# Kernel optimization log

Measured on AMD Instinct MI355X. Metric: run time of the kernel, lower is better.

Reference implementation:

```python
import jax, jax.numpy as jnp
import numpy as np

N_HEAD = 16
D_MODEL = 1024


def setup_inputs() -> dict:
    key = jax.random.key(0)
    ks = jax.random.split(key, 12)
    B, S, D = 2, 2048, D_MODEL
    s = 0.02
    return {
        "q": jax.random.normal(ks[0], (B, S, D), jnp.float32),
        "k": jax.random.normal(ks[1], (B, S, D), jnp.float32),
        "v": jax.random.normal(ks[2], (B, S, 2 * D), jnp.float32),
        "Wq": jax.random.normal(ks[3], (D, D), jnp.float32) * s,
        "bq": jnp.zeros((D,), jnp.float32),
        "Wk": jax.random.normal(ks[4], (D, D), jnp.float32) * s,
        "bk": jnp.zeros((D,), jnp.float32),
        "Wv": jax.random.normal(ks[5], (2 * D, D), jnp.float32) * s,
        "bv": jnp.zeros((D,), jnp.float32),
        "Wfc": jax.random.normal(ks[6], (D, 2 * D), jnp.float32) * s,
        "bfc": jnp.zeros((2 * D,), jnp.float32),
        "padding_mask": jnp.ones((B, S), jnp.int32),
    }


def reference(q, k, v, Wq, bq, Wk, bk, Wv, bv, Wfc, bfc, padding_mask):
    B, S, D = q.shape
    H = N_HEAD
    dh = D // H
    scale = jnp.float32(np.sqrt(dh))
    # projections, split heads -> [B, H, S, dh]
    qh = (q @ Wq + bq).reshape(B, S, H, dh).transpose(0, 2, 1, 3)
    kh = (k @ Wk + bk).reshape(B, S, H, dh).transpose(0, 2, 1, 3)
    vh = (v @ Wv + bv).reshape(B, S, H, dh).transpose(0, 2, 1, 3)
    # scores [B, H, S, S]
    attn = jnp.einsum("bhqd,bhkd->bhqk", qh, kh) / scale
    pad = (padding_mask == 0)[:, None, None, :]  # [B,1,1,S]
    attn = jnp.where(pad, -jnp.inf, attn)
    attn = jax.nn.softmax(attn, axis=-1)
    # dropout p=0 in eval -> identity
    out = jnp.einsum("bhqk,bhkd->bhqd", attn, vh)
    out = out.transpose(0, 2, 1, 3).reshape(B, S, D)
    out = out @ Wfc + bfc  # [B, S, 2D]
    attn_avg = attn.sum(axis=1) / H  # [B, S, S]
    return out, attn_avg
```

## Files before the change

### kernel.cpp

```cpp
#include <hip/hip_runtime.h>
#include <math.h>

#define BATCH   2
#define SLEN    2048
#define DMODEL  1024
#define NHEAD   16
#define DHEAD   64
#define DOUT    2048
#define MROWS   (BATCH * SLEN)
#define NSPLIT  2
#define KSPAN   (SLEN / NSPLIT)

typedef short bf16x8 __attribute__((ext_vector_type(8)));
typedef float floatx4 __attribute__((ext_vector_type(4)));

static __device__ __forceinline__ unsigned short f2bf(float f) {
  unsigned u = __float_as_uint(f);
  u += 0x7fff + ((u >> 16) & 1);
  return (unsigned short)(u >> 16);
}
static __device__ __forceinline__ float bf2f(unsigned short s) {
  return __uint_as_float(((unsigned)s) << 16);
}
static __device__ __forceinline__ unsigned int pk_bf16(float a, float b) {
#if defined(__gfx950__) && __has_builtin(__builtin_amdgcn_cvt_pk_bf16_f32)
  typedef __bf16 bf2_t __attribute__((ext_vector_type(2)));
  bf2_t r = __builtin_amdgcn_cvt_pk_bf16_f32(a, b);
  return __builtin_bit_cast(unsigned int, r);
#else
  return ((unsigned)f2bf(b) << 16) | f2bf(a);
#endif
}
static __device__ __forceinline__ floatx4 mfma16(bf16x8 a, bf16x8 b, floatx4 c) {
  return __builtin_amdgcn_mfma_f32_16x16x32_bf16(a, b, c, 0, 0, 0);
}
static __device__ __forceinline__ void gll16(const void* g, void* l) {
  __builtin_amdgcn_global_load_lds(
      (const __attribute__((address_space(1))) unsigned int*)g,
      (__attribute__((address_space(3))) unsigned int*)l, 16, 0, 0);
}

__global__ __launch_bounds__(256) void conv_all_k(
    const float* __restrict__ q, const float* __restrict__ k,
    const float* __restrict__ v, unsigned short* __restrict__ qb,
    unsigned short* __restrict__ kb, unsigned short* __restrict__ vb) {
  int i = blockIdx.x * 256 + threadIdx.x;
  const float* src;
  unsigned short* dst;
  if (i < (1 << 19)) { src = q; dst = qb; }
  else if (i < (1 << 20)) { src = k; dst = kb; i -= 1 << 19; }
  else { src = v; dst = vb; i -= 1 << 20; }
  const float4 a = ((const float4*)src)[i * 2];
  const float4 b = ((const float4*)src)[i * 2 + 1];
  uint4 u;
  u.x = pk_bf16(a.x, a.y);
  u.y = pk_bf16(a.z, a.w);
  u.z = pk_bf16(b.x, b.y);
  u.w = pk_bf16(b.z, b.w);
  ((uint4*)dst)[i] = u;
}

__global__ __launch_bounds__(256) void wtrans_all_k(
    const float* __restrict__ Wq, const float* __restrict__ Wk,
    const float* __restrict__ Wv, const float* __restrict__ Wfc,
    unsigned short* __restrict__ WqT, unsigned short* __restrict__ WkT,
    unsigned short* __restrict__ WvT, unsigned short* __restrict__ WfcT) {
  __shared__ float T[32][33];
  int id = blockIdx.x;
  const float* W;
  unsigned short* WT;
  int K, N;
  if (id < 1024)      { W = Wq;  WT = WqT;  K = 1024; N = 1024; }
  else if (id < 2048) { W = Wk;  WT = WkT;  K = 1024; N = 1024; id -= 1024; }
  else if (id < 4096) { W = Wv;  WT = WvT;  K = 2048; N = 1024; id -= 2048; }
  else                { W = Wfc; WT = WfcT; K = 1024; N = 2048; id -= 4096; }
  const int ntn = N / 32;
  const int n0 = (id % ntn) * 32, k0 = (id / ntn) * 32;
  const int t = threadIdx.x;
  {
    const int r = t >> 3, c4 = (t & 7) * 4;
    const float4 w = *(const float4*)(W + (size_t)(k0 + r) * N + n0 + c4);
    T[r][c4 + 0] = w.x; T[r][c4 + 1] = w.y; T[r][c4 + 2] = w.z; T[r][c4 + 3] = w.w;
  }
  __syncthreads();
  {
    const int n = t >> 3, k4 = (t & 7) * 4;
    uint2 u;
    u.x = pk_bf16(T[k4 + 0][n], T[k4 + 1][n]);
    u.y = pk_bf16(T[k4 + 2][n], T[k4 + 3][n]);
    *(uint2*)(WT + (size_t)(n0 + n) * K + k0 + k4) = u;
  }
}

template <int MODE>
static __device__ __forceinline__ void gemm_body(
    const unsigned short* __restrict__ A, const unsigned short* __restrict__ BT,
    const float* __restrict__ bias, void* __restrict__ C, int M, int K, int N,
    int row0, int col0) {
  __shared__ unsigned short As[128 * 64];
  __shared__ unsigned short Bs[64 * 64];
  const int t = threadIdx.x;
  const int w = t >> 6, l = t & 63, quad = l >> 4, lq = l & 15;
  const int wm = (w >> 1) * 64, wn = (w & 1) * 32;

  const unsigned short* aS[4];
#pragma unroll
  for (int jj = 0; jj < 4; jj++) {
    const int m = (w * 4 + jj) * 8 + (l >> 3);
    aS[jj] = A + (size_t)(row0 + m) * K + (((l & 7) ^ (m & 7)) << 3);
  }
  const unsigned short* bS[2];
#pragma unroll
  for (int jj = 0; jj < 2; jj++) {
    const int n = (w * 2 + jj) * 8 + (l >> 3);
    bS[jj] = BT + (size_t)(col0 + n) * K + (((l & 7) ^ (n & 7)) << 3);
  }

  floatx4 acc[4][2];
#pragma unroll
  for (int i = 0; i < 4; i++)
#pragma unroll
    for (int j = 0; j < 2; j++) acc[i][j] = (floatx4){0.f, 0.f, 0.f, 0.f};

  for (int kt = 0; kt < K; kt += 64) {
#pragma unroll
    for (int jj = 0; jj < 4; jj++)
      gll16(aS[jj] + kt, As + (w * 4 + jj) * 512);
#pragma unroll
    for (int jj = 0; jj < 2; jj++)
      gll16(bS[jj] + kt, Bs + (w * 2 + jj) * 512);
    __syncthreads();

    bf16x8 af[4][2], bfr[2][2];
#pragma unroll
    for (int ti = 0; ti < 4; ti++) {
      const int m = wm + ti * 16 + lq;
#pragma unroll
      for (int h = 0; h < 2; h++)
        af[ti][h] = *(const bf16x8*)(As + m * 64 + (((h * 4 + quad) ^ (m & 7)) << 3));
    }
#pragma unroll
    for (int tj = 0; tj < 2; tj++) {
      const int n = wn + tj * 16 + lq;
#pragma unroll
      for (int h = 0; h < 2; h++)
        bfr[tj][h] = *(const bf16x8*)(Bs + n * 64 + (((h * 4 + quad) ^ (n & 7)) << 3));
    }
#pragma unroll
    for (int ti = 0; ti < 4; ti++)
#pragma unroll
      for (int tj = 0; tj < 2; tj++) {
        acc[ti][tj] = mfma16(af[ti][0], bfr[tj][0], acc[ti][tj]);
        acc[ti][tj] = mfma16(af[ti][1], bfr[tj][1], acc[ti][tj]);
      }
    __syncthreads();
  }

#pragma unroll
  for (int tj = 0; tj < 2; tj++) {
    const int col = col0 + wn + tj * 16 + lq;
    const float bv = bias[col];
    if (MODE == 2) {
#pragma unroll
      for (int ti = 0; ti < 4; ti++) {
        uint2 u;
        u.x = pk_bf16(acc[ti][tj][0] + bv, acc[ti][tj][1] + bv);
        u.y = pk_bf16(acc[ti][tj][2] + bv, acc[ti][tj][3] + bv);
        *(uint2*)((unsigned short*)C + (size_t)col * M + row0 + wm + ti * 16 +
                  quad * 4) = u;
      }
    } else {
#pragma unroll
      for (int ti = 0; ti < 4; ti++)
#pragma unroll
        for (int r = 0; r < 4; r++) {
          const int row = row0 + wm + ti * 16 + quad * 4 + r;
          const float vv = acc[ti][tj][r] + bv;
          if (MODE == 1)
            ((float*)C)[(size_t)row * N + col] = vv;
          else
            ((unsigned short*)C)[(size_t)row * N + col] = f2bf(vv);
        }
    }
  }
}

__global__ __launch_bounds__(256) void proj_k(
    const unsigned short* qb, const unsigned short* kb, const unsigned short* vb,
    const unsigned short* WqT, const unsigned short* WkT,
    const unsigned short* WvT, const float* bq, const float* bk,
    const float* bv, unsigned short* Qp, unsigned short* Kp,
    unsigned short* VT) {
  const int z = blockIdx.z;
  if (z == 2)
    gemm_body<2>(vb, WvT, bv, VT, MROWS, 2 * DMODEL, DMODEL,
                 blockIdx.y * 128, blockIdx.x * 64);
  else if (z == 1)
    gemm_body<0>(kb, WkT, bk, Kp, MROWS, DMODEL, DMODEL,
                 blockIdx.y * 128, blockIdx.x * 64);
  else
    gemm_body<0>(qb, WqT, bq, Qp, MROWS, DMODEL, DMODEL,
                 blockIdx.y * 128, blockIdx.x * 64);
}
__global__ __launch_bounds__(256) void fc_k(
    const unsigned short* att, const unsigned short* WfcT, const float* bfc,
    float* out) {
  gemm_body<1>(att, WfcT, bfc, out, MROWS, DMODEL, DOUT,
               blockIdx.y * 128, blockIdx.x * 64);
}

__global__ __launch_bounds__(256) void flash_mfma_k(
    const unsigned short* __restrict__ Qp, const unsigned short* __restrict__ Kp,
    const unsigned short* __restrict__ VT, const int* __restrict__ mask,
    unsigned short* __restrict__ Opart, float* __restrict__ Lpart) {
  __shared__ unsigned short Ks[64 * 64];
  __shared__ unsigned short Vs[64 * 64];
  __shared__ unsigned short Ps[4][16 * 68];
  __shared__ float biasL[KSPAN];
  const int t = threadIdx.x;
  const int w = t >> 6, l = t & 63, quad = l >> 4, lq = l & 15;
  const int q0 = blockIdx.x * 64;
  const int h = blockIdx.y >> 1, split = blockIdx.y & 1;
  const int b = blockIdx.z;

  for (int i = t; i < KSPAN; i += 256)
    biasL[i] = mask[b * SLEN + split * KSPAN + i] ? 0.f : -INFINITY;

  const unsigned short* qptr =
      Qp + (size_t)(b * SLEN + q0 + w * 16 + lq) * DMODEL + h * 64;
  const bf16x8 aq0 = *(const bf16x8*)(qptr + quad * 8);
  const bf16x8 aq1 = *(const bf16x8*)(qptr + 32 + quad * 8);

  int krow[2], kchunk[2];
#pragma unroll
  for (int jj = 0; jj < 2; jj++) {
    krow[jj] = (w * 2 + jj) * 8 + (l >> 3);
    kchunk[jj] = (l & 7) ^ (krow[jj] & 7);
  }
  const unsigned short* Kbase = Kp + (size_t)b * SLEN * DMODEL + h * 64;
  const unsigned short* Vbase = VT + (size_t)h * 64 * MROWS + b * SLEN;

  floatx4 acc_o[4];
#pragma unroll
  for (int dj = 0; dj < 4; dj++) acc_o[dj] = (floatx4){0.f, 0.f, 0.f, 0.f};
  float lsum = 0.f;
  unsigned short* PsW = &Ps[w][0];

  for (int k0s = 0; k0s < KSPAN; k0s += 64) {
    const int k0 = split * KSPAN + k0s;
    __syncthreads();
#pragma unroll
    for (int jj = 0; jj < 2; jj++) {
      const int inst = w * 2 + jj;
      gll16(Kbase + (size_t)(k0 + krow[jj]) * DMODEL + kchunk[jj] * 8,
            Ks + inst * 512);
      gll16(Vbase + (size_t)krow[jj] * MROWS + k0 + kchunk[jj] * 8,
            Vs + inst * 512);
    }
    __syncthreads();

#pragma unroll
    for (int ti = 0; ti < 4; ti++) {
      const int kk = ti * 16 + lq;
      const bf16x8 bk0 = *(const bf16x8*)(Ks + kk * 64 + ((quad ^ (kk & 7)) << 3));
      const bf16x8 bk1 =
          *(const bf16x8*)(Ks + kk * 64 + (((4 + quad) ^ (kk & 7)) << 3));
      floatx4 z = (floatx4){0.f, 0.f, 0.f, 0.f};
      z = mfma16(bk0, aq0, z);
      z = mfma16(bk1, aq1, z);
      const float4 bb = *(const float4*)&biasL[k0s + ti * 16 + quad * 4];
      const float e0 = __expf(fmaf(z[0], 0.125f, bb.x));
      const float e1 = __expf(fmaf(z[1], 0.125f, bb.y));
      const float e2 = __expf(fmaf(z[2], 0.125f, bb.z));
      const float e3 = __expf(fmaf(z[3], 0.125f, bb.w));
      lsum += (e0 + e1) + (e2 + e3);
      uint2 pk;
      pk.x = pk_bf16(e0, e1);
      pk.y = pk_bf16(e2, e3);
      *(uint2*)(PsW + lq * 68 + ti * 16 + quad * 4) = pk;
    }
    __asm__ __volatile__("" ::: "memory");
    const bf16x8 ap0 = *(const bf16x8*)(PsW + lq * 68 + quad * 8);
    const bf16x8 ap1 = *(const bf16x8*)(PsW + lq * 68 + 32 + quad * 8);
#pragma unroll
    for (int dj = 0; dj < 4; dj++) {
      const int d = dj * 16 + lq;
      const bf16x8 bv0 = *(const bf16x8*)(Vs + d * 64 + ((quad ^ (d & 7)) << 3));
      const bf16x8 bv1 =
          *(const bf16x8*)(Vs + d * 64 + (((4 + quad) ^ (d & 7)) << 3));
      acc_o[dj] = mfma16(ap0, bv0, acc_o[dj]);
      acc_o[dj] = mfma16(ap1, bv1, acc_o[dj]);
    }
  }

  lsum += __shfl_xor(lsum, 16);
  lsum += __shfl_xor(lsum, 32);

  const size_t obase =
      (((size_t)split * BATCH + b) * NHEAD + h) * SLEN + q0 + w * 16;
#pragma unroll
  for (int dj = 0; dj < 4; dj++)
#pragma unroll
    for (int r = 0; r < 4; r++)
      Opart[(obase + quad * 4 + r) * DHEAD + dj * 16 + lq] = f2bf(acc_o[dj][r]);
  if (quad == 0) Lpart[obase + lq] = lsum;
}

__global__ __launch_bounds__(256) void combine_k(
    const unsigned short* __restrict__ Opart, const float* __restrict__ Lpart,
    unsigned short* __restrict__ att, float* __restrict__ lbuf) {
  const int gid = blockIdx.x * 256 + threadIdx.x;
  const int row = gid >> 3;
  const int d8 = (gid & 7) * 8;
  const float l0 = Lpart[row];
  const float l1 = Lpart[(size_t)BATCH * NHEAD * SLEN + row];
  const float lt = l0 + l1;
  const float il = (lt > 0.f) ? 1.f / lt : 0.f;
  const bf16x8 o0 = *(const bf16x8*)(Opart + (size_t)row * DHEAD + d8);
  const bf16x8 o1 = *(const bf16x8*)(Opart + (size_t)(BATCH * NHEAD * SLEN) * DHEAD +
                                     (size_t)row * DHEAD + d8);
  const int b = row >> 15, hh = (row >> 11) & 15, q = row & 2047;
  unsigned short* dst = att + (size_t)(b * SLEN + q) * DMODEL + hh * 64 + d8;
  float vv[8];
#pragma unroll
  for (int j = 0; j < 8; j++)
    vv[j] = (bf2f((unsigned short)o0[j]) + bf2f((unsigned short)o1[j])) * il;
  uint4 u;
  u.x = pk_bf16(vv[0], vv[1]);
  u.y = pk_bf16(vv[2], vv[3]);
  u.z = pk_bf16(vv[4], vv[5]);
  u.w = pk_bf16(vv[6], vv[7]);
  *(uint4*)dst = u;
  if ((gid & 7) == 0) lbuf[row] = lt;
}

__global__ __launch_bounds__(256) void attn_avg_mfma_k(
    const unsigned short* __restrict__ Qp, const unsigned short* __restrict__ Kp,
    const float* __restrict__ lbuf, const int* __restrict__ mask,
    float* __restrict__ aout) {
  __shared__ unsigned short Ks[64 * 64];
  __shared__ float ilL[NHEAD * 64];
  const int t = threadIdx.x;
  const int w = t >> 6, l = t & 63, quad = l >> 4, lq = l & 15;
  const int k0 = blockIdx.x * 64, q0 = blockIdx.y * 64, b = blockIdx.z;

  for (int i = t; i < NHEAD * 64; i += 256) {
    const float lv = lbuf[(b * NHEAD + (i >> 6)) * SLEN + q0 + (i & 63)];
    ilL[i] = (lv > 0.f) ? 1.f / lv : 0.f;
  }
  float bb[4];
#pragma unroll
  for (int ti = 0; ti < 4; ti++)
    bb[ti] = mask[b * SLEN + k0 + ti * 16 + lq] ? 0.f : -INFINITY;

  floatx4 acc[4];
#pragma unroll
  for (int ti = 0; ti < 4; ti++) acc[ti] = (floatx4){0.f, 0.f, 0.f, 0.f};

  int krow[2], kchunk[2];
#pragma unroll
  for (int jj = 0; jj < 2; jj++) {
    krow[jj] = (w * 2 + jj) * 8 + (l >> 3);
    kchunk[jj] = (l & 7) ^ (krow[jj] & 7);
  }
  const unsigned short* Kbase = Kp + (size_t)(b * SLEN + k0) * DMODEL;
  const unsigned short* qbase =
      Qp + (size_t)(b * SLEN + q0 + w * 16 + lq) * DMODEL;

  for (int h = 0; h < NHEAD; h++) {
    __syncthreads();
#pragma unroll
    for (int jj = 0; jj < 2; jj++)
      gll16(Kbase + (size_t)krow[jj] * DMODEL + h * 64 + kchunk[jj] * 8,
            Ks + (w * 2 + jj) * 512);
    __syncthreads();

    const bf16x8 aq0 = *(const bf16x8*)(qbase + h * 64 + quad * 8);
    const bf16x8 aq1 = *(const bf16x8*)(qbase + h * 64 + 32 + quad * 8);
    const float4 il4 = *(const float4*)&ilL[h * 64 + w * 16 + quad * 4];
    const float ila[4] = {il4.x, il4.y, il4.z, il4.w};
#pragma unroll
    for (int ti = 0; ti < 4; ti++) {
      const int kk = ti * 16 + lq;
      const bf16x8 bk0 = *(const bf16x8*)(Ks + kk * 64 + ((quad ^ (kk & 7)) << 3));
      const bf16x8 bk1 =
          *(const bf16x8*)(Ks + kk * 64 + (((4 + quad) ^ (kk & 7)) << 3));
      floatx4 z = (floatx4){0.f, 0.f, 0.f, 0.f};
      z = mfma16(aq0, bk0, z);
      z = mfma16(aq1, bk1, z);
#pragma unroll
      for (int r = 0; r < 4; r++)
        acc[ti][r] = fmaf(__expf(fmaf(z[r], 0.125f, bb[ti])), ila[r], acc[ti][r]);
    }
  }
  const float ih = 1.f / NHEAD;
#pragma unroll
  for (int ti = 0; ti < 4; ti++)
#pragma unroll
    for (int r = 0; r < 4; r++)
      aout[(size_t)(b * SLEN + q0 + w * 16 + quad * 4 + r) * SLEN + k0 +
           ti * 16 + lq] = acc[ti][r] * ih;
}

extern "C" void kernel_launch(void* const* d_in, const int* in_sizes, int n_in,
                              void* d_out, int out_size, void* d_ws, size_t ws_size,
                              hipStream_t stream) {
  const float* q   = (const float*)d_in[0];
  const float* k   = (const float*)d_in[1];
  const float* v   = (const float*)d_in[2];
  const float* Wq  = (const float*)d_in[3];
  const float* bq  = (const float*)d_in[4];
  const float* Wk  = (const float*)d_in[5];
  const float* bk  = (const float*)d_in[6];
  const float* Wv  = (const float*)d_in[7];
  const float* bv  = (const float*)d_in[8];
  const float* Wfc = (const float*)d_in[9];
  const float* bfc = (const float*)d_in[10];
  const int* mask  = (const int*)d_in[11];

  float* out      = (float*)d_out;
  float* attn_avg = out + (size_t)MROWS * DOUT;

  unsigned short* qb = (unsigned short*)d_out;
  unsigned short* kb = qb + (1u << 22);
  unsigned short* vb = kb + (1u << 22);
  unsigned short* Opart = (unsigned short*)d_out;
  float* Lpart = (float*)((char*)d_out + (size_t)NSPLIT * BATCH * NHEAD * SLEN * DHEAD * 2);

  unsigned short* wsb  = (unsigned short*)d_ws;
  unsigned short* WqT  = wsb;
  unsigned short* WkT  = wsb + (1u << 20);
  unsigned short* WvT  = wsb + (2u << 20);
  unsigned short* WfcT = wsb + (4u << 20);
  unsigned short* Qp   = wsb + (6u << 20);
  unsigned short* Kp   = Qp + (1u << 22);
  unsigned short* VT   = Kp + (1u << 22);
  unsigned short* att  = VT + (1u << 22);
  float* lbuf = (float*)(att + (1u << 22));

  conv_all_k<<<dim3(8192), dim3(256), 0, stream>>>(q, k, v, qb, kb, vb);
  wtrans_all_k<<<dim3(6144), dim3(256), 0, stream>>>(Wq, Wk, Wv, Wfc,
                                                     WqT, WkT, WvT, WfcT);
  proj_k<<<dim3(DMODEL / 64, MROWS / 128, 3), dim3(256), 0, stream>>>(
      qb, kb, vb, WqT, WkT, WvT, bq, bk, bv, Qp, Kp, VT);
  flash_mfma_k<<<dim3(SLEN / 64, NHEAD * NSPLIT, BATCH), dim3(256), 0, stream>>>(
      Qp, Kp, VT, mask, Opart, Lpart);
  combine_k<<<dim3(BATCH * NHEAD * SLEN * DHEAD / 8 / 256), dim3(256), 0, stream>>>(
      Opart, Lpart, att, lbuf);
  attn_avg_mfma_k<<<dim3(SLEN / 64, SLEN / 64, BATCH), dim3(256), 0, stream>>>(
      Qp, Kp, lbuf, mask, attn_avg);
  fc_k<<<dim3(DOUT / 64, MROWS / 128), dim3(256), 0, stream>>>(
      att, WfcT, bfc, out);
}
```

Measured before the change: 367.2 us.

## Enlarge GEMM and flash tiles, fold softmax scale into Q, use exp2

The GEMM tile grows from 128x64 to 128x128, giving each wave a 64x64 sub-tile with more MFMA work per LDS load. The flash kernel now handles 128 queries per block, so each K/V tile loaded is reused across two query sub-tiles per wave. The 1/sqrt(dh)*log2(e) scale is folded into the Q projection epilogue so both attention kernels can call exp2f directly without a multiply. The attention-average kernel loads K for two heads per barrier pair, halving synchronisations. Costs are higher register and LDS use, which may reduce occupancy, and fewer blocks in the grids.

```diff
diff --git a/kernel.cpp b/kernel.cpp
--- a/kernel.cpp
+++ b/kernel.cpp
@@ -10,6 +10,7 @@
 #define MROWS   (BATCH * SLEN)
 #define NSPLIT  2
 #define KSPAN   (SLEN / NSPLIT)
+#define QSCALE  0.1803368801f
 
 typedef short bf16x8 __attribute__((ext_vector_type(8)));
 typedef float floatx4 __attribute__((ext_vector_type(4)));
@@ -96,60 +97,51 @@
 static __device__ __forceinline__ void gemm_body(
     const unsigned short* __restrict__ A, const unsigned short* __restrict__ BT,
     const float* __restrict__ bias, void* __restrict__ C, int M, int K, int N,
-    int row0, int col0) {
+    int row0, int col0, float scale) {
   __shared__ unsigned short As[128 * 64];
-  __shared__ unsigned short Bs[64 * 64];
+  __shared__ unsigned short Bs[128 * 64];
   const int t = threadIdx.x;
   const int w = t >> 6, l = t & 63, quad = l >> 4, lq = l & 15;
-  const int wm = (w >> 1) * 64, wn = (w & 1) * 32;
-
-  const unsigned short* aS[4];
+  const int wm = (w >> 1) * 64, wn = (w & 1) * 64;
+
+  const unsigned short *aS[4], *bS[4];
 #pragma unroll
   for (int jj = 0; jj < 4; jj++) {
-    const int m = (w * 4 + jj) * 8 + (l >> 3);
-    aS[jj] = A + (size_t)(row0 + m) * K + (((l & 7) ^ (m & 7)) << 3);
-  }
-  const unsigned short* bS[2];
-#pragma unroll
-  for (int jj = 0; jj < 2; jj++) {
-    const int n = (w * 2 + jj) * 8 + (l >> 3);
-    bS[jj] = BT + (size_t)(col0 + n) * K + (((l & 7) ^ (n & 7)) << 3);
-  }
-
-  floatx4 acc[4][2];
+    const int r = (w * 4 + jj) * 8 + (l >> 3);
+    const int c = ((l & 7) ^ (r & 7)) << 3;
+    aS[jj] = A + (size_t)(row0 + r) * K + c;
+    bS[jj] = BT + (size_t)(col0 + r) * K + c;
+  }
+
+  floatx4 acc[4][4];
 #pragma unroll
   for (int i = 0; i < 4; i++)
 #pragma unroll
-    for (int j = 0; j < 2; j++) acc[i][j] = (floatx4){0.f, 0.f, 0.f, 0.f};
+    for (int j = 0; j < 4; j++) acc[i][j] = (floatx4){0.f, 0.f, 0.f, 0.f};
 
   for (int kt = 0; kt < K; kt += 64) {
 #pragma unroll
-    for (int jj = 0; jj < 4; jj++)
+    for (int jj = 0; jj < 4; jj++) {
       gll16(aS[jj] + kt, As + (w * 4 + jj) * 512);
-#pragma unroll
-    for (int jj = 0; jj < 2; jj++)
-      gll16(bS[jj] + kt, Bs + (w * 2 + jj) * 512);
-    __syncthreads();
-
-    bf16x8 af[4][2], bfr[2][2];
+      gll16(bS[jj] + kt, Bs + (w * 4 + jj) * 512);
+    }
+    __syncthreads();
+
+    bf16x8 af[4][2], bfr[4][2];
 #pragma unroll
     for (int ti = 0; ti < 4; ti++) {
       const int m = wm + ti * 16 + lq;
-#pragma unroll
-      for (int h = 0; h < 2; h++)
+      const int n = wn + ti * 16 + lq;
+#pragma unroll
+      for (int h = 0; h < 2; h++) {
         af[ti][h] = *(const bf16x8*)(As + m * 64 + (((h * 4 + quad) ^ (m & 7)) << 3));
-    }
-#pragma unroll
-    for (int tj = 0; tj < 2; tj++) {
-      const int n = wn + tj * 16 + lq;
-#pragma unroll
-      for (int h = 0; h < 2; h++)
-        bfr[tj][h] = *(const bf16x8*)(Bs + n * 64 + (((h * 4 + quad) ^ (n & 7)) << 3));
+        bfr[ti][h] = *(const bf16x8*)(Bs + n * 64 + (((h * 4 + quad) ^ (n & 7)) << 3));
+      }
     }
 #pragma unroll
     for (int ti = 0; ti < 4; ti++)
 #pragma unroll
-      for (int tj = 0; tj < 2; tj++) {
+      for (int tj = 0; tj < 4; tj++) {
         acc[ti][tj] = mfma16(af[ti][0], bfr[tj][0], acc[ti][tj]);
         acc[ti][tj] = mfma16(af[ti][1], bfr[tj][1], acc[ti][tj]);
       }
@@ -157,15 +149,15 @@
   }
 
 #pragma unroll
-  for (int tj = 0; tj < 2; tj++) {
+  for (int tj = 0; tj < 4; tj++) {
     const int col = col0 + wn + tj * 16 + lq;
     const float bv = bias[col];
     if (MODE == 2) {
 #pragma unroll
       for (int ti = 0; ti < 4; ti++) {
         uint2 u;
-        u.x = pk_bf16(acc[ti][tj][0] + bv, acc[ti][tj][1] + bv);
-        u.y = pk_bf16(acc[ti][tj][2] + bv, acc[ti][tj][3] + bv);
+        u.x = pk_bf16((acc[ti][tj][0] + bv) * scale, (acc[ti][tj][1] + bv) * scale);
+        u.y = pk_bf16((acc[ti][tj][2] + bv) * scale, (acc[ti][tj][3] + bv) * scale);
         *(uint2*)((unsigned short*)C + (size_t)col * M + row0 + wm + ti * 16 +
                   quad * 4) = u;
       }
@@ -175,7 +167,7 @@
 #pragma unroll
         for (int r = 0; r < 4; r++) {
           const int row = row0 + wm + ti * 16 + quad * 4 + r;
-          const float vv = acc[ti][tj][r] + bv;
+          const float vv = (acc[ti][tj][r] + bv) * scale;
           if (MODE == 1)
             ((float*)C)[(size_t)row * N + col] = vv;
           else
@@ -194,19 +186,19 @@
   const int z = blockIdx.z;
   if (z == 2)
     gemm_body<2>(vb, WvT, bv, VT, MROWS, 2 * DMODEL, DMODEL,
-                 blockIdx.y * 128, blockIdx.x * 64);
+                 blockIdx.y * 128, blockIdx.x * 128, 1.f);
   else if (z == 1)
     gemm_body<0>(kb, WkT, bk, Kp, MROWS, DMODEL, DMODEL,
-                 blockIdx.y * 128, blockIdx.x * 64);
+                 blockIdx.y * 128, blockIdx.x * 128, 1.f);
   else
     gemm_body<0>(qb, WqT, bq, Qp, MROWS, DMODEL, DMODEL,
-                 blockIdx.y * 128, blockIdx.x * 64);
+                 blockIdx.y * 128, blockIdx.x * 128, QSCALE);
 }
 __global__ __launch_bounds__(256) void fc_k(
     const unsigned short* att, const unsigned short* WfcT, const float* bfc,
     float* out) {
   gemm_body<1>(att, WfcT, bfc, out, MROWS, DMODEL, DOUT,
-               blockIdx.y * 128, blockIdx.x * 64);
+               blockIdx.y * 128, blockIdx.x * 128, 1.f);
 }
 
 __global__ __launch_bounds__(256) void flash_mfma_k(
@@ -215,21 +207,25 @@
     unsigned short* __restrict__ Opart, float* __restrict__ Lpart) {
   __shared__ unsigned short Ks[64 * 64];
   __shared__ unsigned short Vs[64 * 64];
-  __shared__ unsigned short Ps[4][16 * 68];
+  __shared__ unsigned short Ps[4][32 * 68];
   __shared__ float biasL[KSPAN];
   const int t = threadIdx.x;
   const int w = t >> 6, l = t & 63, quad = l >> 4, lq = l & 15;
-  const int q0 = blockIdx.x * 64;
+  const int q0 = blockIdx.x * 128;
   const int h = blockIdx.y >> 1, split = blockIdx.y & 1;
   const int b = blockIdx.z;
 
   for (int i = t; i < KSPAN; i += 256)
     biasL[i] = mask[b * SLEN + split * KSPAN + i] ? 0.f : -INFINITY;
 
-  const unsigned short* qptr =
-      Qp + (size_t)(b * SLEN + q0 + w * 16 + lq) * DMODEL + h * 64;
-  const bf16x8 aq0 = *(const bf16x8*)(qptr + quad * 8);
-  const bf16x8 aq1 = *(const bf16x8*)(qptr + 32 + quad * 8);
+  bf16x8 aq[2][2];
+#pragma unroll
+  for (int s = 0; s < 2; s++) {
+    const unsigned short* qptr =
+        Qp + (size_t)(b * SLEN + q0 + w * 32 + s * 16 + lq) * DMODEL + h * 64;
+    aq[s][0] = *(const bf16x8*)(qptr + quad * 8);
+    aq[s][1] = *(const bf16x8*)(qptr + 32 + quad * 8);
+  }
 
   int krow[2], kchunk[2];
 #pragma unroll
@@ -240,10 +236,12 @@
   const unsigned short* Kbase = Kp + (size_t)b * SLEN * DMODEL + h * 64;
   const unsigned short* Vbase = VT + (size_t)h * 64 * MROWS + b * SLEN;
 
-  floatx4 acc_o[4];
-#pragma unroll
-  for (int dj = 0; dj < 4; dj++) acc_o[dj] = (floatx4){0.f, 0.f, 0.f, 0.f};
-  float lsum = 0.f;
+  floatx4 acc_o[2][4];
+#pragma unroll
+  for (int s = 0; s < 2; s++)
+#pragma unroll
+    for (int dj = 0; dj < 4; dj++) acc_o[s][dj] = (floatx4){0.f, 0.f, 0.f, 0.f};
+  float lsum[2] = {0.f, 0.f};
   unsigned short* PsW = &Ps[w][0];
 
   for (int k0s = 0; k0s < KSPAN; k0s += 64) {
@@ -265,45 +263,61 @@
       const bf16x8 bk0 = *(const bf16x8*)(Ks + kk * 64 + ((quad ^ (kk & 7)) << 3));
       const bf16x8 bk1 =
           *(const bf16x8*)(Ks + kk * 64 + (((4 + quad) ^ (kk & 7)) << 3));
-      floatx4 z = (floatx4){0.f, 0.f, 0.f, 0.f};
-      z = mfma16(bk0, aq0, z);
-      z = mfma16(bk1, aq1, z);
       const float4 bb = *(const float4*)&biasL[k0s + ti * 16 + quad * 4];
-      const float e0 = __expf(fmaf(z[0], 0.125f, bb.x));
-      const float e1 = __expf(fmaf(z[1], 0.125f, bb.y));
-      const float e2 = __expf(fmaf(z[2], 0.125f, bb.z));
-      const float e3 = __expf(fmaf(z[3], 0.125f, bb.w));
-      lsum += (e0 + e1) + (e2 + e3);
-      uint2 pk;
-      pk.x = pk_bf16(e0, e1);
-      pk.y = pk_bf16(e2, e3);
-      *(uint2*)(PsW + lq * 68 + ti * 16 + quad * 4) = pk;
+#pragma unroll
+      for (int s = 0; s < 2; s++) {
+        floatx4 z = (floatx4){0.f, 0.f, 0.f, 0.f};
+        z = mfma16(bk0, aq[s][0], z);
+        z = mfma16(bk1, aq[s][1], z);
+        const float e0 = exp2f(z[0] + bb.x);
+        const float e1 = exp2f(z[1] + bb.y);
+        const float e2 = exp2f(z[2] + bb.z);
+        const float e3 = exp2f(z[3] + bb.w);
+        lsum[s] += (e0 + e1) + (e2 + e3);
+        uint2 pk;
+        pk.x = pk_bf16(e0, e1);
+        pk.y = pk_bf16(e2, e3);
+        *(uint2*)(PsW + (s * 16 + lq) * 68 + ti * 16 + quad * 4) = pk;
+      }
     }
     __asm__ __volatile__("" ::: "memory");
-    const bf16x8 ap0 = *(const bf16x8*)(PsW + lq * 68 + quad * 8);
-    const bf16x8 ap1 = *(const bf16x8*)(PsW + lq * 68 + 32 + quad * 8);
-#pragma unroll
-    for (int dj = 0; dj < 4; dj++) {
-      const int d = dj * 16 + lq;
-      const bf16x8 bv0 = *(const bf16x8*)(Vs + d * 64 + ((quad ^ (d & 7)) << 3));
-      const bf16x8 bv1 =
-          *(const bf16x8*)(Vs + d * 64 + (((4 + quad) ^ (d & 7)) << 3));
-      acc_o[dj] = mfma16(ap0, bv0, acc_o[dj]);
-      acc_o[dj] = mfma16(ap1, bv1, acc_o[dj]);
-    }
-  }
-
-  lsum += __shfl_xor(lsum, 16);
-  lsum += __shfl_xor(lsum, 32);
+#pragma unroll
+    for (int s = 0; s < 2; s++) {
+      const bf16x8 ap0 = *(const bf16x8*)(PsW + (s * 16 + lq) * 68 + quad * 8);
+      const bf16x8 ap1 =
+          *(const bf16x8*)(PsW + (s * 16 + lq) * 68 + 32 + quad * 8);
+#pragma unroll
+      for (int dj = 0; dj < 4; dj++) {
+        const int d = dj * 16 + lq;
+        const bf16x8 bv0 = *(const bf16x8*)(Vs + d * 64 + ((quad ^ (d & 7)) << 3));
+        const bf16x8 bv1 =
+            *(const bf16x8*)(Vs + d * 64 + (((4 + quad) ^ (d & 7)) << 3));
+        acc_o[s][dj] = mfma16(ap0, bv0, acc_o[s][dj]);
+        acc_o[s][dj] = mfma16(ap1, bv1, acc_o[s][dj]);
+      }
+    }
+  }
+
+#pragma unroll
+  for (int s = 0; s < 2; s++) {
+    float v = lsum[s];
+    v += __shfl_xor(v, 16);
+    v += __shfl_xor(v, 32);
+    lsum[s] = v;
+  }
 
   const size_t obase =
-      (((size_t)split * BATCH + b) * NHEAD + h) * SLEN + q0 + w * 16;
-#pragma unroll
-  for (int dj = 0; dj < 4; dj++)
-#pragma unroll
-    for (int r = 0; r < 4; r++)
-      Opart[(obase + quad * 4 + r) * DHEAD + dj * 16 + lq] = f2bf(acc_o[dj][r]);
-  if (quad == 0) Lpart[obase + lq] = lsum;
+      (((size_t)split * BATCH + b) * NHEAD + h) * SLEN + q0 + w * 32;
+#pragma unroll
+  for (int s = 0; s < 2; s++) {
+#pragma unroll
+    for (int dj = 0; dj < 4; dj++)
+#pragma unroll
+      for (int r = 0; r < 4; r++)
+        Opart[(obase + s * 16 + quad * 4 + r) * DHEAD + dj * 16 + lq] =
+            f2bf(acc_o[s][dj][r]);
+    if (quad == 0) Lpart[obase + s * 16 + lq] = lsum[s];
+  }
 }
 
 __global__ __launch_bounds__(256) void combine_k(
@@ -338,7 +352,7 @@
     const unsigned short* __restrict__ Qp, const unsigned short* __restrict__ Kp,
     const float* __restrict__ lbuf, const int* __restrict__ mask,
     float* __restrict__ aout) {
-  __shared__ unsigned short Ks[64 * 64];
+  __shared__ unsigned short Ks[2][64 * 64];
   __shared__ float ilL[NHEAD * 64];
   const int t = threadIdx.x;
   const int w = t >> 6, l = t & 63, quad = l >> 4, lq = l & 15;
@@ -367,30 +381,37 @@
   const unsigned short* qbase =
       Qp + (size_t)(b * SLEN + q0 + w * 16 + lq) * DMODEL;
 
-  for (int h = 0; h < NHEAD; h++) {
-    __syncthreads();
-#pragma unroll
-    for (int jj = 0; jj < 2; jj++)
-      gll16(Kbase + (size_t)krow[jj] * DMODEL + h * 64 + kchunk[jj] * 8,
-            Ks + (w * 2 + jj) * 512);
-    __syncthreads();
-
-    const bf16x8 aq0 = *(const bf16x8*)(qbase + h * 64 + quad * 8);
-    const bf16x8 aq1 = *(const bf16x8*)(qbase + h * 64 + 32 + quad * 8);
-    const float4 il4 = *(const float4*)&ilL[h * 64 + w * 16 + quad * 4];
-    const float ila[4] = {il4.x, il4.y, il4.z, il4.w};
-#pragma unroll
-    for (int ti = 0; ti < 4; ti++) {
-      const int kk = ti * 16 + lq;
-      const bf16x8 bk0 = *(const bf16x8*)(Ks + kk * 64 + ((quad ^ (kk & 7)) << 3));
-      const bf16x8 bk1 =
-          *(const bf16x8*)(Ks + kk * 64 + (((4 + quad) ^ (kk & 7)) << 3));
-      floatx4 z = (floatx4){0.f, 0.f, 0.f, 0.f};
-      z = mfma16(aq0, bk0, z);
-      z = mfma16(aq1, bk1, z);
-#pragma unroll
-      for (int r = 0; r < 4; r++)
-        acc[ti][r] = fmaf(__expf(fmaf(z[r], 0.125f, bb[ti])), ila[r], acc[ti][r]);
+  for (int hp = 0; hp < NHEAD; hp += 2) {
+    __syncthreads();
+#pragma unroll
+    for (int p = 0; p < 2; p++)
+#pragma unroll
+      for (int jj = 0; jj < 2; jj++)
+        gll16(Kbase + (size_t)krow[jj] * DMODEL + (hp + p) * 64 + kchunk[jj] * 8,
+              Ks[p] + (w * 2 + jj) * 512);
+    __syncthreads();
+
+#pragma unroll
+    for (int p = 0; p < 2; p++) {
+      const int h = hp + p;
+      const bf16x8 aq0 = *(const bf16x8*)(qbase + h * 64 + quad * 8);
+      const bf16x8 aq1 = *(const bf16x8*)(qbase + h * 64 + 32 + quad * 8);
+      const float4 il4 = *(const float4*)&ilL[h * 64 + w * 16 + quad * 4];
+      const float ila[4] = {il4.x, il4.y, il4.z, il4.w};
+#pragma unroll
+      for (int ti = 0; ti < 4; ti++) {
+        const int kk = ti * 16 + lq;
+        const bf16x8 bk0 =
+            *(const bf16x8*)(Ks[p] + kk * 64 + ((quad ^ (kk & 7)) << 3));
+        const bf16x8 bk1 =
+            *(const bf16x8*)(Ks[p] + kk * 64 + (((4 + quad) ^ (kk & 7)) << 3));
+        floatx4 z = (floatx4){0.f, 0.f, 0.f, 0.f};
+        z = mfma16(aq0, bk0, z);
+        z = mfma16(aq1, bk1, z);
+#pragma unroll
+        for (int r = 0; r < 4; r++)
+          acc[ti][r] = fmaf(exp2f(z[r] + bb[ti]), ila[r], acc[ti][r]);
+      }
     }
   }
   const float ih = 1.f / NHEAD;
@@ -441,14 +462,14 @@
   conv_all_k<<<dim3(8192), dim3(256), 0, stream>>>(q, k, v, qb, kb, vb);
   wtrans_all_k<<<dim3(6144), dim3(256), 0, stream>>>(Wq, Wk, Wv, Wfc,
                                                      WqT, WkT, WvT, WfcT);
-  proj_k<<<dim3(DMODEL / 64, MROWS / 128, 3), dim3(256), 0, stream>>>(
+  proj_k<<<dim3(DMODEL / 128, MROWS / 128, 3), dim3(256), 0, stream>>>(
       qb, kb, vb, WqT, WkT, WvT, bq, bk, bv, Qp, Kp, VT);
-  flash_mfma_k<<<dim3(SLEN / 64, NHEAD * NSPLIT, BATCH), dim3(256), 0, stream>>>(
+  flash_mfma_k<<<dim3(SLEN / 128, NHEAD * NSPLIT, BATCH), dim3(256), 0, stream>>>(
       Qp, Kp, VT, mask, Opart, Lpart);
   combine_k<<<dim3(BATCH * NHEAD * SLEN * DHEAD / 8 / 256), dim3(256), 0, stream>>>(
       Opart, Lpart, att, lbuf);
   attn_avg_mfma_k<<<dim3(SLEN / 64, SLEN / 64, BATCH), dim3(256), 0, stream>>>(
       Qp, Kp, lbuf, mask, attn_avg);
-  fc_k<<<dim3(DOUT / 64, MROWS / 128), dim3(256), 0, stream>>>(
+  fc_k<<<dim3(DOUT / 128, MROWS / 128), dim3(256), 0, stream>>>(
       att, WfcT, bfc, out);
 }
```

After: 378.4 us. +3.1%, slower.
